# Performance work log

Hardware: AMD Instinct MI355X
Metric: run time of the kernel (lower is better)

Reference implementation:

```python
import jax, jax.numpy as jnp
import numpy as np

N_NODES = 50000
N_EDGES = 800000
N_FEAT = 128
HIDDEN = 128
N_CLASSES = 10
N_LAYERS = 3
N_GRAPHS = 512


def setup_inputs() -> dict:
    key = jax.random.key(0)
    ks = jax.random.split(key, 16)
    s = 1.0 / np.sqrt(HIDDEN)
    inp = {
        "x": jax.random.normal(ks[0], (N_NODES, N_FEAT), jnp.float32),
        "edge_index": jax.random.randint(ks[1], (2, N_EDGES), 0, N_NODES, jnp.int64),
        "batch": jnp.sort(jax.random.randint(ks[2], (N_NODES,), 0, N_GRAPHS, jnp.int64)),
        "num_graphs": N_GRAPHS,
        "conv1_wl": jax.random.normal(ks[3], (N_FEAT, HIDDEN), jnp.float32) * s,
        "conv1_wr": jax.random.normal(ks[4], (N_FEAT, HIDDEN), jnp.float32) * s,
        "conv1_b": jnp.zeros((HIDDEN,), jnp.float32),
        "convs_wl": jax.random.normal(ks[5], (N_LAYERS - 1, HIDDEN, HIDDEN), jnp.float32) * s,
        "convs_wr": jax.random.normal(ks[6], (N_LAYERS - 1, HIDDEN, HIDDEN), jnp.float32) * s,
        "convs_b": jnp.zeros((N_LAYERS - 1, HIDDEN), jnp.float32),
        "gate_w": jax.random.normal(ks[7], (HIDDEN, 1), jnp.float32) * s,
        "gate_b": jnp.zeros((1,), jnp.float32),
        "lin1_w": jax.random.normal(ks[8], (HIDDEN, HIDDEN), jnp.float32) * s,
        "lin1_b": jnp.zeros((HIDDEN,), jnp.float32),
        "lin2_w": jax.random.normal(ks[9], (HIDDEN, N_CLASSES), jnp.float32) * s,
        "lin2_b": jnp.zeros((N_CLASSES,), jnp.float32),
    }
    return inp


def _sage_conv(x, src, dst, inv_deg, wl, wr, b):
    # mean aggregation of source-node features at destination nodes
    agg = jax.ops.segment_sum(x[src], dst, num_segments=N_NODES)  # [N, d]
    agg = agg * inv_deg
    return agg @ wl + x @ wr + b


def _global_attention(x, batch, num_graphs, gate_w, gate_b):
    gate = (x @ gate_w + gate_b)[:, 0]                      # [N]
    m = jax.ops.segment_max(gate, batch, num_segments=num_graphs)
    m = jnp.where(jnp.isfinite(m), m, 0.0)
    g = jnp.exp(gate - m[batch])                            # stable segment softmax
    den = jax.ops.segment_sum(g, batch, num_segments=num_graphs)
    attn = g / den[batch]
    return jax.ops.segment_sum(attn[:, None] * x, batch, num_segments=num_graphs)


def reference(x, edge_index, batch, num_graphs,
              conv1_wl, conv1_wr, conv1_b,
              convs_wl, convs_wr, convs_b,
              gate_w, gate_b, lin1_w, lin1_b, lin2_w, lin2_b):
    src, dst = edge_index[0], edge_index[1]
    deg = jax.ops.segment_sum(jnp.ones((src.shape[0],), x.dtype), dst,
                              num_segments=N_NODES)
    inv_deg = (1.0 / jnp.maximum(deg, 1.0))[:, None]

    h = jax.nn.relu(_sage_conv(x, src, dst, inv_deg, conv1_wl, conv1_wr, conv1_b))
    for i in range(convs_wl.shape[0]):
        h = jax.nn.relu(_sage_conv(h, src, dst, inv_deg,
                                   convs_wl[i], convs_wr[i], convs_b[i]))

    pooled = _global_attention(h, batch, num_graphs, gate_w, gate_b)  # [G, H]
    out = jax.nn.relu(pooled @ lin1_w + lin1_b)
    # dropout p=0.5 is identity at eval time
    logits = out @ lin2_w + lin2_b
    return jax.nn.log_softmax(logits, axis=-1)
```

## Files before the change

### kernel.cpp

```cpp
#include <hip/hip_runtime.h>
#include <math.h>

#define N_NODES 50000
#define N_PAD   50048
#define N_EDGES 800000
#define FEAT 128
#define K2 256
#define N_GRAPHS 512
#define N_CLASSES 10
#define BCAP 64
#define BROW 264
#define OROW 72
#define AGG_BLOCKS 2048
#define CNT_STRIDE 16

#define FILLB 3125
#define PREP_BLOCKS (FILLB + 6250 + 384 + 3)

typedef __attribute__((ext_vector_type(8))) short short8;
typedef __attribute__((ext_vector_type(4))) float floatx4;

__device__ __forceinline__ float bflo(unsigned u) { return __uint_as_float(u << 16); }
__device__ __forceinline__ float bfhi(unsigned u) { return __uint_as_float(u & 0xffff0000u); }
__device__ __forceinline__ unsigned short f2bf(float f) {
    unsigned u = __float_as_uint(f);
    u = (u + 0x7fffu + ((u >> 16) & 1u)) >> 16;
    return (unsigned short)u;
}
__device__ __forceinline__ unsigned pack2(float a, float b) {
    return (unsigned)f2bf(a) | ((unsigned)f2bf(b) << 16);
}

__global__ __launch_bounds__(256) void prep_kernel(
    const int* __restrict__ src, const int* __restrict__ dst,
    int* __restrict__ cnt, unsigned short* __restrict__ bucket,
    const float* __restrict__ x, unsigned short* __restrict__ A,
    const float* __restrict__ wl1, const float* __restrict__ wr1,
    const float* __restrict__ wl23, const float* __restrict__ wr23,
    unsigned short* __restrict__ wt,
    const int* __restrict__ batch, int* __restrict__ goffs) {
    int b = blockIdx.x, t = threadIdx.x;
    if (b < FILLB) {
        int e = b * 256 + t;
        int d = dst[e];
        int p = atomicAdd(&cnt[d << 4], 1);
        if (p < BCAP) bucket[(size_t)d * BCAP + p] = (unsigned short)src[e];
    } else if (b < FILLB + 6250) {
        int idx = (b - FILLB) * 256 + t;
        if (idx < N_NODES * 32) {
            int n = idx >> 5, f4 = idx & 31;
            float4 v = ((const float4*)(x + (size_t)n * FEAT))[f4];
            uint2 o = make_uint2(pack2(v.x, v.y), pack2(v.z, v.w));
            *(uint2*)(A + (size_t)n * K2 + FEAT + f4 * 4) = o;
        }
    } else if (b < FILLB + 6250 + 384) {
        int idx = (b - FILLB - 6250) * 256 + t;
        int layer = idx >> 15;
        int r = idx & 32767;
        int n = r >> 8, k = r & 255;
        const float* wl = (layer == 0) ? wl1 : wl23 + (size_t)(layer - 1) * FEAT * FEAT;
        const float* wr = (layer == 0) ? wr1 : wr23 + (size_t)(layer - 1) * FEAT * FEAT;
        float v = (k < FEAT) ? wl[k * FEAT + n] : wr[(k - FEAT) * FEAT + n];
        wt[idx] = f2bf(v);
    } else {
        int g = (b - FILLB - 6250 - 384) * 256 + t;
        if (g > N_GRAPHS) return;
        int lo = 0, hi = N_NODES;
        while (lo < hi) {
            int mid = (lo + hi) >> 1;
            if (batch[mid] < g) lo = mid + 1; else hi = mid;
        }
        goffs[g] = lo;
    }
}

__device__ __forceinline__ void acc8(float* acc, uint4 u) {
    acc[0] += bflo(u.x); acc[1] += bfhi(u.x);
    acc[2] += bflo(u.y); acc[3] += bfhi(u.y);
    acc[4] += bflo(u.z); acc[5] += bfhi(u.z);
    acc[6] += bflo(u.w); acc[7] += bfhi(u.w);
}

__global__ __launch_bounds__(256) void aggregate_bf16(
    const unsigned short* __restrict__ hin, const int* __restrict__ cnt,
    const unsigned short* __restrict__ bucket, unsigned short* __restrict__ aggout) {
    int lane = threadIdx.x & 63;
    int g = lane >> 4;
    int l16 = lane & 15;
    int wid = (blockIdx.x << 2) + (threadIdx.x >> 6);
    const int nw = gridDim.x << 2;

    int n = wid;
    if (n >= N_NODES) return;
    int deg = cnt[n << 4];

    while (true) {
        const unsigned short* cp = bucket + (size_t)n * BCAP;
        int c = min(deg, BCAP);
        int nq = c >> 2;
        int rem = c & 3;

        int nn = n + nw;
        int dnext = 0;
        if (nn < N_NODES) {
            dnext = cnt[nn << 4];
            unsigned short bpre = bucket[(size_t)nn * BCAP + lane];
            asm volatile("" :: "v"((int)bpre));
        }

        float acc[8];
        #pragma unroll
        for (int i = 0; i < 8; ++i) acc[i] = 0.f;

        int i = 0;
        for (; i + 4 <= nq; i += 4) {
            int s0 = cp[i * 4 + g];
            int s1 = cp[i * 4 + 4 + g];
            int s2 = cp[i * 4 + 8 + g];
            int s3 = cp[i * 4 + 12 + g];
            uint4 u0 = *(const uint4*)(hin + (size_t)s0 * K2 + l16 * 8);
            uint4 u1 = *(const uint4*)(hin + (size_t)s1 * K2 + l16 * 8);
            uint4 u2 = *(const uint4*)(hin + (size_t)s2 * K2 + l16 * 8);
            uint4 u3 = *(const uint4*)(hin + (size_t)s3 * K2 + l16 * 8);
            acc8(acc, u0); acc8(acc, u1); acc8(acc, u2); acc8(acc, u3);
        }
        if (i + 2 <= nq) {
            int s0 = cp[i * 4 + g];
            int s1 = cp[i * 4 + 4 + g];
            uint4 u0 = *(const uint4*)(hin + (size_t)s0 * K2 + l16 * 8);
            uint4 u1 = *(const uint4*)(hin + (size_t)s1 * K2 + l16 * 8);
            acc8(acc, u0); acc8(acc, u1);
            i += 2;
        }
        if (i < nq) {
            int s0 = cp[i * 4 + g];
            uint4 u0 = *(const uint4*)(hin + (size_t)s0 * K2 + l16 * 8);
            acc8(acc, u0);
        }
        if (g < rem) {
            int s0 = cp[nq * 4 + g];
            uint4 u0 = *(const uint4*)(hin + (size_t)s0 * K2 + l16 * 8);
            acc8(acc, u0);
        }
        #pragma unroll
        for (int j = 0; j < 8; ++j) {
            acc[j] += __shfl_xor(acc[j], 16);
            acc[j] += __shfl_xor(acc[j], 32);
        }
        if (g == 0) {
            float inv = 1.0f / fmaxf((float)deg, 1.0f);
            uint4 o;
            o.x = pack2(acc[0] * inv, acc[1] * inv);
            o.y = pack2(acc[2] * inv, acc[3] * inv);
            o.z = pack2(acc[4] * inv, acc[5] * inv);
            o.w = pack2(acc[6] * inv, acc[7] * inv);
            *(uint4*)(aggout + (size_t)n * K2 + l16 * 8) = o;
        }
        if (nn >= N_NODES) break;
        n = nn;
        deg = dnext;
    }
}

__global__ __launch_bounds__(256, 4) void gemm_mfma(
    const unsigned short* __restrict__ Ain, unsigned short* __restrict__ Aout,
    const unsigned short* __restrict__ Wt, const float* __restrict__ bias,
    const float* __restrict__ gate_w, float* __restrict__ gate) {
    __shared__ __align__(16) char smem[64 * BROW * 2];
    unsigned short* sB = (unsigned short*)smem;
    unsigned short* sOutW;
    int t = threadIdx.x;
    int wave = t >> 6, lane = t & 63;
    int q = lane >> 4, l16 = lane & 15;
    sOutW = (unsigned short*)smem + wave * 32 * OROW;

    const int nwg_q = 97, nwg_r = 6;
    int orig = blockIdx.x;
    int xcd = orig & 7, idx = orig >> 3;
    int wgid = (xcd < nwg_r) ? xcd * (nwg_q + 1) + idx
                             : nwg_r * (nwg_q + 1) + (xcd - nwg_r) * nwg_q + idx;
    int tileM = wgid >> 1;
    int nh = wgid & 1;
    int row0 = tileM * 128 + wave * 32;

    const unsigned short* pa0 = Ain + (size_t)(row0 + l16) * K2 + q * 8;
    const unsigned short* pa1 = pa0 + 16 * K2;
    short8 a0[8], a1[8];
    #pragma unroll
    for (int ks = 0; ks < 8; ++ks) {
        a0[ks] = *(const short8*)(pa0 + ks * 32);
        a1[ks] = *(const short8*)(pa1 + ks * 32);
    }

    #pragma unroll
    for (int i = 0; i < 8; ++i) {
        int flat = i * 256 + t;
        int rw = flat >> 5, fr = flat & 31;
        uint4 v = *((const uint4*)(Wt + (size_t)(nh * 64 + rw) * K2) + fr);
        *(uint4*)(&sB[rw * BROW + fr * 8]) = v;
    }
    __syncthreads();

    floatx4 acc[2][4];
    #pragma unroll
    for (int i = 0; i < 2; ++i)
        #pragma unroll
        for (int j = 0; j < 4; ++j) acc[i][j] = (floatx4){0.f, 0.f, 0.f, 0.f};

    #pragma unroll
    for (int ks = 0; ks < 8; ++ks) {
        #pragma unroll
        for (int nb = 0; nb < 4; ++nb) {
            short8 b = *(const short8*)(&sB[(nb * 16 + l16) * BROW + ks * 32 + q * 8]);
            acc[0][nb] = __builtin_amdgcn_mfma_f32_16x16x32_bf16(a0[ks], b, acc[0][nb], 0, 0, 0);
            acc[1][nb] = __builtin_amdgcn_mfma_f32_16x16x32_bf16(a1[ks], b, acc[1][nb], 0, 0, 0);
        }
    }
    __syncthreads();

    float bv[4], gwv[4];
    #pragma unroll
    for (int nb = 0; nb < 4; ++nb) bv[nb] = bias[nh * 64 + nb * 16 + l16];
    if (gate_w) {
        #pragma unroll
        for (int nb = 0; nb < 4; ++nb) gwv[nb] = gate_w[nh * 64 + nb * 16 + l16];
    }

    #pragma unroll
    for (int band = 0; band < 2; ++band) {
        #pragma unroll
        for (int r = 0; r < 4; ++r) {
            int lr = band * 16 + q * 4 + r;
            float gsum = 0.f;
            #pragma unroll
            for (int nb = 0; nb < 4; ++nb) {
                float v = fmaxf(acc[band][nb][r] + bv[nb], 0.f);
                sOutW[lr * OROW + nb * 16 + l16] = f2bf(v);
                if (gate_w) gsum += v * gwv[nb];
            }
            if (gate_w) {
                gsum += __shfl_xor(gsum, 1);
                gsum += __shfl_xor(gsum, 2);
                gsum += __shfl_xor(gsum, 4);
                gsum += __shfl_xor(gsum, 8);
                int m = row0 + lr;
                if (l16 == 0 && m < N_NODES) atomicAdd(&gate[m], gsum);
            }
        }
    }

    int r2 = lane >> 1, h2 = lane & 1;
    size_t gbase = (size_t)(row0 + r2) * K2 + FEAT + nh * 64 + h2 * 32;
    #pragma unroll
    for (int j = 0; j < 2; ++j) {
        uint4 v0 = *(uint4*)(&sOutW[r2 * OROW + h2 * 32 + j * 16]);
        uint4 v1 = *(uint4*)(&sOutW[r2 * OROW + h2 * 32 + j * 16 + 8]);
        *(uint4*)(Aout + gbase + j * 16) = v0;
        *(uint4*)(Aout + gbase + j * 16 + 8) = v1;
    }
}

__global__ __launch_bounds__(256) void pool_head(
    const unsigned short* __restrict__ h, const float* __restrict__ gate,
    const int* __restrict__ goffs,
    const float* __restrict__ w1, const float* __restrict__ b1,
    const float* __restrict__ w2, const float* __restrict__ b2,
    float* __restrict__ out) {
    __shared__ float sred[4];
    __shared__ float facc[4][128];
    __shared__ float pv[128], qv[128], lg[N_CLASSES];
    int g = blockIdx.x;
    int s = goffs[g], e = goffs[g + 1];
    int t = threadIdx.x;
    int wave = t >> 6, lane = t & 63;

    if (s < e) {
        float mx = -INFINITY;
        for (int n = s + t; n < e; n += 256) mx = fmaxf(mx, gate[n]);
        #pragma unroll
        for (int off = 32; off; off >>= 1) mx = fmaxf(mx, __shfl_xor(mx, off));
        if (lane == 0) sred[wave] = mx;
        __syncthreads();
        float m = fmaxf(fmaxf(sred[0], sred[1]), fmaxf(sred[2], sred[3]));
        __syncthreads();
        float d = 0.f;
        for (int n = s + t; n < e; n += 256) d += __expf(gate[n] - m);
        #pragma unroll
        for (int off = 32; off; off >>= 1) d += __shfl_xor(d, off);
        if (lane == 0) sred[wave] = d;
        __syncthreads();
        float den = sred[0] + sred[1] + sred[2] + sred[3];
        float acc0 = 0.f, acc1 = 0.f;
        for (int n = s + wave; n < e; n += 4) {
            float gn = __expf(gate[n] - m);
            unsigned u = *(const unsigned*)(h + (size_t)n * K2 + lane * 2);
            acc0 += gn * bflo(u);
            acc1 += gn * bfhi(u);
        }
        facc[wave][lane * 2]     = acc0;
        facc[wave][lane * 2 + 1] = acc1;
        __syncthreads();
        if (t < 128) pv[t] = (facc[0][t] + facc[1][t] + facc[2][t] + facc[3][t]) / den;
    } else {
        if (t < 128) pv[t] = 0.f;
    }
    __syncthreads();

    if (t < 128) {
        float acc = b1[t];
        #pragma unroll 4
        for (int k = 0; k < 128; ++k) acc += pv[k] * w1[k * FEAT + t];
        qv[t] = fmaxf(acc, 0.f);
    }
    __syncthreads();
    if (t < N_CLASSES) {
        float a = b2[t];
        #pragma unroll 4
        for (int k = 0; k < 128; ++k) a += qv[k] * w2[k * N_CLASSES + t];
        lg[t] = a;
    }
    __syncthreads();
    if (t < N_CLASSES) {
        float m = -INFINITY;
        #pragma unroll
        for (int j = 0; j < N_CLASSES; ++j) m = fmaxf(m, lg[j]);
        float sum = 0.f;
        #pragma unroll
        for (int j = 0; j < N_CLASSES; ++j) sum += __expf(lg[j] - m);
        out[(size_t)g * N_CLASSES + t] = lg[t] - m - __logf(sum);
    }
}

static inline size_t align256(size_t x) { return (x + 255) & ~(size_t)255; }

extern "C" void kernel_launch(void* const* d_in, const int* in_sizes, int n_in,
                              void* d_out, int out_size, void* d_ws, size_t ws_size,
                              hipStream_t stream) {
    const float* x        = (const float*)d_in[0];
    const int*   ei       = (const int*)d_in[1];
    const int*   batch    = (const int*)d_in[2];
    const float* conv1_wl = (const float*)d_in[4];
    const float* conv1_wr = (const float*)d_in[5];
    const float* conv1_b  = (const float*)d_in[6];
    const float* convs_wl = (const float*)d_in[7];
    const float* convs_wr = (const float*)d_in[8];
    const float* convs_b  = (const float*)d_in[9];
    const float* gate_w   = (const float*)d_in[10];
    const float* lin1_w   = (const float*)d_in[12];
    const float* lin1_b   = (const float*)d_in[13];
    const float* lin2_w   = (const float*)d_in[14];
    const float* lin2_b   = (const float*)d_in[15];
    float* out = (float*)d_out;

    const int* src = ei;
    const int* dst = ei + N_EDGES;

    char* w = (char*)d_ws;
    size_t off = 0;
    unsigned short* A0   = (unsigned short*)(w + off); off += align256((size_t)N_PAD * K2 * 2);
    unsigned short* A1   = (unsigned short*)(w + off); off += align256((size_t)N_PAD * K2 * 2);
    unsigned short* bkt  = (unsigned short*)(w + off); off += align256((size_t)N_NODES * BCAP * 2);
    unsigned short* wt   = (unsigned short*)(w + off); off += align256((size_t)3 * FEAT * K2 * 2);
    int*   i_goff = (int*)(w + off);   off += align256((size_t)(N_GRAPHS + 1) * 4);
    char* zbase = w + off;
    int*   i_cnt  = (int*)(w + off);   off += align256((size_t)N_NODES * CNT_STRIDE * 4);
    float* f_gate = (float*)(w + off); off += align256((size_t)N_NODES * 4);
    size_t zbytes = (size_t)((w + off) - zbase);

    hipMemsetAsync(zbase, 0, zbytes, stream);

    prep_kernel<<<PREP_BLOCKS, 256, 0, stream>>>(
        src, dst, i_cnt, bkt,
        x, A0, conv1_wl, conv1_wr, convs_wl, convs_wr, wt, batch, i_goff);

    const int GB = (N_PAD / 128) * 2;

    aggregate_bf16<<<AGG_BLOCKS, 256, 0, stream>>>(A0 + FEAT, i_cnt, bkt, A0);
    gemm_mfma<<<GB, 256, 0, stream>>>(A0, A1, wt, conv1_b, nullptr, nullptr);
    aggregate_bf16<<<AGG_BLOCKS, 256, 0, stream>>>(A1 + FEAT, i_cnt, bkt, A1);
    gemm_mfma<<<GB, 256, 0, stream>>>(A1, A0, wt + FEAT * K2, convs_b, nullptr, nullptr);
    aggregate_bf16<<<AGG_BLOCKS, 256, 0, stream>>>(A0 + FEAT, i_cnt, bkt, A0);
    gemm_mfma<<<GB, 256, 0, stream>>>(A0, A1, wt + 2 * FEAT * K2, convs_b + FEAT,
                                      gate_w, f_gate);

    pool_head<<<N_GRAPHS, 256, 0, stream>>>(A1 + FEAT, f_gate, i_goff,
                                            lin1_w, lin1_b, lin2_w, lin2_b, out);
}
```

Measured before the change: 302.7 us.

## Partition aggregation nodes by XCD and split GEMM output LDS from weight tile

The aggregation kernel now gives each XCD (selected by blockIdx & 7) a contiguous range of node IDs, matching the GEMM's XCD tile mapping, instead of striding all waves across the whole node set. The aim is better L2 locality between the aggregate output and the GEMM that reads it, and within each XCD's work. The GEMM also gives the output staging buffer its own shared memory instead of aliasing the B tile, which removes one __syncthreads but raises LDS use per block, and the occupancy hint in launch_bounds is dropped. Blocks in one XCD get fixed node ranges regardless of degree, which may unbalance load.

```diff
diff --git a/kernel.cpp b/kernel.cpp
--- a/kernel.cpp
+++ b/kernel.cpp
@@ -29,6 +29,14 @@
 }
 __device__ __forceinline__ unsigned pack2(float a, float b) {
     return (unsigned)f2bf(a) | ((unsigned)f2bf(b) << 16);
+}
+
+__device__ __forceinline__ void xcd_range(int x, int& lo, int& hi) {
+    int S = (x < 6) ? 98 * x : (x == 6 ? 588 : 685);
+    int C = (x < 6) ? 98 : 97;
+    lo = S * 64;
+    hi = (S + C) * 64;
+    if (hi > N_NODES) hi = N_NODES;
 }
 
 __global__ __launch_bounds__(256) void prep_kernel(
@@ -87,11 +95,15 @@
     int lane = threadIdx.x & 63;
     int g = lane >> 4;
     int l16 = lane & 15;
-    int wid = (blockIdx.x << 2) + (threadIdx.x >> 6);
-    const int nw = gridDim.x << 2;
-
-    int n = wid;
-    if (n >= N_NODES) return;
+    int x = blockIdx.x & 7;
+    int w = ((blockIdx.x >> 3) << 2) + (threadIdx.x >> 6);
+    const int nw = (AGG_BLOCKS >> 3) << 2;
+
+    int lo, hi;
+    xcd_range(x, lo, hi);
+
+    int n = lo + w;
+    if (n >= hi) return;
     int deg = cnt[n << 4];
 
     while (true) {
@@ -102,7 +114,7 @@
 
         int nn = n + nw;
         int dnext = 0;
-        if (nn < N_NODES) {
+        if (nn < hi) {
             dnext = cnt[nn << 4];
             unsigned short bpre = bucket[(size_t)nn * BCAP + lane];
             asm volatile("" :: "v"((int)bpre));
@@ -156,23 +168,21 @@
             o.w = pack2(acc[6] * inv, acc[7] * inv);
             *(uint4*)(aggout + (size_t)n * K2 + l16 * 8) = o;
         }
-        if (nn >= N_NODES) break;
+        if (nn >= hi) break;
         n = nn;
         deg = dnext;
     }
 }
 
-__global__ __launch_bounds__(256, 4) void gemm_mfma(
+__global__ __launch_bounds__(256) void gemm_mfma(
     const unsigned short* __restrict__ Ain, unsigned short* __restrict__ Aout,
     const unsigned short* __restrict__ Wt, const float* __restrict__ bias,
     const float* __restrict__ gate_w, float* __restrict__ gate) {
-    __shared__ __align__(16) char smem[64 * BROW * 2];
-    unsigned short* sB = (unsigned short*)smem;
-    unsigned short* sOutW;
+    __shared__ unsigned short sB[64 * BROW];
+    __shared__ unsigned short sOut[4][32 * OROW];
     int t = threadIdx.x;
     int wave = t >> 6, lane = t & 63;
     int q = lane >> 4, l16 = lane & 15;
-    sOutW = (unsigned short*)smem + wave * 32 * OROW;
 
     const int nwg_q = 97, nwg_r = 6;
     int orig = blockIdx.x;
@@ -216,7 +226,6 @@
             acc[1][nb] = __builtin_amdgcn_mfma_f32_16x16x32_bf16(a1[ks], b, acc[1][nb], 0, 0, 0);
         }
     }
-    __syncthreads();
 
     float bv[4], gwv[4];
     #pragma unroll
@@ -235,7 +244,7 @@
             #pragma unroll
             for (int nb = 0; nb < 4; ++nb) {
                 float v = fmaxf(acc[band][nb][r] + bv[nb], 0.f);
-                sOutW[lr * OROW + nb * 16 + l16] = f2bf(v);
+                sOut[wave][lr * OROW + nb * 16 + l16] = f2bf(v);
                 if (gate_w) gsum += v * gwv[nb];
             }
             if (gate_w) {
@@ -253,8 +262,8 @@
     size_t gbase = (size_t)(row0 + r2) * K2 + FEAT + nh * 64 + h2 * 32;
     #pragma unroll
     for (int j = 0; j < 2; ++j) {
-        uint4 v0 = *(uint4*)(&sOutW[r2 * OROW + h2 * 32 + j * 16]);
-        uint4 v1 = *(uint4*)(&sOutW[r2 * OROW + h2 * 32 + j * 16 + 8]);
+        uint4 v0 = *(uint4*)(&sOut[wave][r2 * OROW + h2 * 32 + j * 16]);
+        uint4 v1 = *(uint4*)(&sOut[wave][r2 * OROW + h2 * 32 + j * 16 + 8]);
         *(uint4*)(Aout + gbase + j * 16) = v0;
         *(uint4*)(Aout + gbase + j * 16 + 8) = v1;
     }
```

Measured after the change: 300.5 us. About the same (-0.7%).
